# Performance work log

Measured on AMD Instinct MI355X. Metric: run time of the kernel, lower is better.

Reference implementation:

```python
import jax, jax.numpy as jnp
import numpy as np

B, S, D, H, E, TOPK = 8, 1024, 512, 2048, 8, 2


def setup_inputs() -> dict:
    key = jax.random.key(0)
    ks = jax.random.split(key, 7)
    scale = 0.02
    return {
        "x": jax.random.normal(ks[0], (B, S, D), jnp.float32),
        "gate_w": jax.random.normal(ks[1], (D, E), jnp.float32) * scale,
        "gate_b": jnp.zeros((E,), jnp.float32),
        "w1": jax.random.normal(ks[2], (E, D, H), jnp.float32) * scale,
        "b1": jnp.zeros((E, H), jnp.float32),
        "w2": jax.random.normal(ks[3], (E, H, D), jnp.float32) * scale,
        "b2": jnp.zeros((E, D), jnp.float32),
    }


def reference(x, gate_w, gate_b, w1, b1, w2, b2):
    # ---- MoE transformer MLP (fastmoe FMoETransformerMLP, NaiveGate) ----
    xt = x.reshape(-1, D)                       # [T, D], T = B*S tokens
    logits = xt @ gate_w + gate_b               # [T, E]
    top_val, top_idx = jax.lax.top_k(logits, TOPK)  # [T, k]
    score = jax.nn.softmax(top_val, axis=-1)    # softmax over the k selected logits

    y = jnp.zeros_like(xt)
    # Loop over the small fixed expert set; each token's combine weight for
    # expert e is the sum of its top-k scores routed to e (0 if not selected).
    for e in range(E):
        w_tok = jnp.sum(score * (top_idx == e), axis=-1)        # [T]
        h = jax.nn.gelu(xt @ w1[e] + b1[e], approximate=False)  # [T, H]
        y = y + w_tok[:, None] * (h @ w2[e] + b2[e])            # [T, D]

    y = y.reshape(B, S, D)
    # Outer model: log_softmax over seq of channel-summed features
    return jax.nn.log_softmax(jnp.sum(y, axis=2), axis=1)       # [B, S]
```

## Files before the change

kernel.cpp:

```cpp
#include <hip/hip_runtime.h>
#include <hip/hip_bf16.h>
#include <math.h>

#define T_TOK 8192
#define DIM   512
#define NEXP  8
#define HID   2048
#define NBAT  8
#define SEQ   1024

typedef short  short8 __attribute__((ext_vector_type(8)));
typedef float  f32x4  __attribute__((ext_vector_type(4)));

__device__ __forceinline__ unsigned short f2bf(float f) {
    union { float f; unsigned int u; } v; v.f = f;
    unsigned int u = v.u;
    unsigned int r = u + 0x7FFFu + ((u >> 16) & 1u);
    return (unsigned short)(r >> 16);
}

__device__ __forceinline__ float gelu_f(float v) {
    float v2 = v * v;
    float w = v * (-2.302344f - 0.102955f * v2);
    return v / (1.f + __builtin_amdgcn_exp2f(w));
}

__global__ void prep_gate_k(const float* __restrict__ w1, unsigned short* __restrict__ w1f,
                            const float* __restrict__ w2, const float* __restrict__ b2,
                            float* __restrict__ w2sum, float* __restrict__ b2sum,
                            int* __restrict__ counts,
                            const float* __restrict__ x, const float* __restrict__ gw,
                            const float* __restrict__ gb,
                            unsigned short* __restrict__ xb,
                            int* __restrict__ eidx, float* __restrict__ esc0,
                            float* __restrict__ esc1) {
    int bid = blockIdx.x;
    int tid = threadIdx.x;
    int wave = tid >> 6, lane = tid & 63;
    if (bid < 2048) {
        __shared__ unsigned short tile[64][68];
        int e = bid >> 8, r = bid & 255;
        int d0 = (r & 7) * 64, h0 = (r >> 3) * 64;
        const float* src = w1 + (size_t)e * DIM * HID;
        #pragma unroll
        for (int pass = 0; pass < 4; ++pass) {
            int dr = pass * 16 + (tid >> 4);
            int hc = (tid & 15) * 4;
            float4 v = *(const float4*)(src + (size_t)(d0 + dr) * HID + h0 + hc);
            tile[hc + 0][dr] = f2bf(v.x);
            tile[hc + 1][dr] = f2bf(v.y);
            tile[hc + 2][dr] = f2bf(v.z);
            tile[hc + 3][dr] = f2bf(v.w);
        }
        __syncthreads();
        int l = tid & 63, q = l >> 4, c = l & 15;
        int kk0 = (r & 7) * 2, g0 = (r >> 3) * 4;
        #pragma unroll
        for (int pi = 0; pi < 2; ++pi) {
            int sub = pi * 4 + wave;
            int kk2 = sub >> 2, g2 = sub & 3;
            const unsigned short* tp = &tile[g2 * 16 + c][kk2 * 32 + q * 8];
            ushort4 a = *(const ushort4*)(tp);
            ushort4 b = *(const ushort4*)(tp + 4);
            unsigned short* dst = w1f +
                ((size_t)(e * 128 + g0 + g2) * 16 + kk0 + kk2) * 512 + l * 8;
            *(ushort4*)(dst)     = a;
            *(ushort4*)(dst + 4) = b;
        }
    } else if (bid < 4096) {
        int t = (bid - 2048) * 4 + wave;
        const float* xp = x + (size_t)t * DIM;
        unsigned short* xbp = xb + (size_t)t * DIM;
        float acc[8] = {0, 0, 0, 0, 0, 0, 0, 0};
        #pragma unroll
        for (int it = 0; it < 8; ++it) {
            int d = it * 64 + lane;
            float xv = xp[d];
            xbp[d] = f2bf(xv);
            float4 g0 = *(const float4*)(gw + d * 8);
            float4 g1 = *(const float4*)(gw + d * 8 + 4);
            acc[0] += xv * g0.x; acc[1] += xv * g0.y; acc[2] += xv * g0.z; acc[3] += xv * g0.w;
            acc[4] += xv * g1.x; acc[5] += xv * g1.y; acc[6] += xv * g1.z; acc[7] += xv * g1.w;
        }
        #pragma unroll
        for (int e = 0; e < 8; ++e) {
            float s = acc[e];
            #pragma unroll
            for (int off = 32; off >= 1; off >>= 1) s += __shfl_xor(s, off);
            acc[e] = s + gb[e];
        }
        float v0 = -1e30f, v1 = -1e30f; int i0 = 0, i1 = 0;
        #pragma unroll
        for (int e = 0; e < 8; ++e) {
            float v = acc[e];
            if (v > v0) { v1 = v0; i1 = i0; v0 = v; i0 = e; }
            else if (v > v1) { v1 = v; i1 = e; }
        }
        float e1 = expf(v1 - v0);
        float inv = 1.f / (1.f + e1);
        if (lane == 0) {
            eidx[t] = i0 | (i1 << 4);
            esc0[t] = inv;
            esc1[t] = e1 * inv;
        }
    } else if (bid < 8192) {
        int row = (bid - 4096) * 4 + wave;
        const float* p = w2 + (size_t)row * DIM;
        float4 a = *(const float4*)(p + lane * 4);
        float4 b = *(const float4*)(p + 256 + lane * 4);
        float s = a.x + a.y + a.z + a.w + b.x + b.y + b.z + b.w;
        #pragma unroll
        for (int off = 32; off >= 1; off >>= 1) s += __shfl_xor(s, off);
        if (lane == 0) w2sum[row] = s;
    } else {
        if (tid < 8) counts[tid] = 0;
        for (int r = wave; r < NEXP; r += 4) {
            const float* p = b2 + (size_t)r * DIM;
            float s = 0.f;
            for (int i = lane; i < DIM; i += 64) s += p[i];
            #pragma unroll
            for (int off = 32; off >= 1; off >>= 1) s += __shfl_xor(s, off);
            if (lane == 0) b2sum[r] = s;
        }
    }
}

__global__ __launch_bounds__(1024) void route_k(
    const int* __restrict__ eidx, const float* __restrict__ esc0,
    const float* __restrict__ esc1, const float* __restrict__ b2sum,
    int* __restrict__ counts,
    int* __restrict__ ptok, float* __restrict__ pscore,
    float* __restrict__ s_partial) {
    int tid = threadIdx.x;
    int t = blockIdx.x * 1024 + tid;
    int wv = tid >> 6, lane = tid & 63;
    int pk = eidx[t];
    int i0 = pk & 0xf, i1 = (pk >> 4) & 0xf;
    float s0 = esc0[t], s1 = esc1[t];

    s_partial[t] = s0 * b2sum[i0] + s1 * b2sum[i1];

    __shared__ int waveCnt[16][8];
    __shared__ int waveBase[16][8];

    unsigned long long m0[8], m1[8];
    #pragma unroll
    for (int e = 0; e < 8; ++e) {
        m0[e] = __ballot(i0 == e);
        m1[e] = __ballot(i1 == e);
    }
    if (lane < 8) {
        int c = 0;
        #pragma unroll
        for (int e = 0; e < 8; ++e)
            if (lane == e) c = __popcll(m0[e]) + __popcll(m1[e]);
        waveCnt[wv][lane] = c;
    }
    __syncthreads();
    if (tid < 8) {
        int e = tid;
        int total = 0;
        #pragma unroll
        for (int w = 0; w < 16; ++w) total += waveCnt[w][e];
        int base = atomicAdd(&counts[e], total);
        int run = base;
        #pragma unroll
        for (int w = 0; w < 16; ++w) {
            waveBase[w][e] = run;
            run += waveCnt[w][e];
        }
    }
    __syncthreads();

    unsigned long long lt = (1ULL << lane) - 1ULL;
    int slot0 = 0, slot1 = 0;
    #pragma unroll
    for (int e = 0; e < 8; ++e) {
        if (i0 == e) slot0 = waveBase[wv][e] + __popcll(m0[e] & lt);
        if (i1 == e) slot1 = waveBase[wv][e] + __popcll(m0[e]) + __popcll(m1[e] & lt);
    }
    ptok[i0 * T_TOK + slot0] = t;  pscore[i0 * T_TOK + slot0] = s0;
    ptok[i1 * T_TOK + slot1] = t;  pscore[i1 * T_TOK + slot1] = s1;
}

#define GPTR(p) (const __attribute__((address_space(1))) void*)(p)
#define LPTR(p) (__attribute__((address_space(3))) void*)(p)

__global__ __launch_bounds__(256, 3) void moe_gemm_k(
    const unsigned short* __restrict__ xb, const unsigned short* __restrict__ w1f,
    const float* __restrict__ b1, const float* __restrict__ w2sum,
    const int* __restrict__ counts, const int* __restrict__ ptok,
    const float* __restrict__ pscore, float* __restrict__ s_partial) {

    int flat = blockIdx.x + (int)blockIdx.y * 135;
    int xcd = flat & 7;
    int s = flat >> 3;
    int bx = s >> 1;
    int hBase = (xcd * 2 + (s & 1)) * 128;

    int e = 8, rowBase = 0, accT = 0;
    #pragma unroll
    for (int i = 0; i < 8; ++i) {
        int nt = (counts[i] + 127) >> 7;
        if (e == 8 && bx < accT + nt) { e = i; rowBase = (bx - accT) * 128; }
        accT += nt;
    }
    if (e == 8) return;
    int n_e = counts[e];

    __shared__ unsigned short A_s[2][128 * 64];
    __shared__ int   tokLds[128];
    __shared__ float scoreLds[128];

    int tid = threadIdx.x;
    int wave = tid >> 6, lane = tid & 63;

    if (tid < 128) {
        int r = rowBase + tid;
        bool valid = r < n_e;
        tokLds[tid]   = valid ? ptok[e * T_TOK + r]   : 0;
        scoreLds[tid] = valid ? pscore[e * T_TOK + r] : 0.f;
    }
    __syncthreads();

    unsigned gAo[4];
    #pragma unroll
    for (int i = 0; i < 4; ++i) {
        int c = i * 256 + tid;
        int row = c >> 3, pos = c & 7;
        int j = (pos ^ (row & 7)) * 8;
        gAo[i] = (unsigned)tokLds[row] * DIM + j;
    }

    int wm = wave >> 1, wn = wave & 1;
    int quad = lane >> 4, col = lane & 15;

    f32x4 acc[4][4];
    #pragma unroll
    for (int m = 0; m < 4; ++m)
        #pragma unroll
        for (int n = 0; n < 4; ++n)
            acc[m][n] = (f32x4){0.f, 0.f, 0.f, 0.f};

    int aOff0 = (wm * 64 + col) * 64 + ((((0 << 2) | quad) ^ (col & 7)) * 8);
    int aOff1 = (wm * 64 + col) * 64 + ((((1 << 2) | quad) ^ (col & 7)) * 8);

    const unsigned short* bp = w1f +
        (size_t)(e * 128 + (hBase >> 4) + wn * 4) * 8192 + lane * 8;
    short8 bf0[4], bf1[4];

    #pragma unroll
    for (int i = 0; i < 4; ++i)
        __builtin_amdgcn_global_load_lds(GPTR(xb + gAo[i]), LPTR(&A_s[0][i * 2048 + tid * 8]), 16, 0, 0);
    __builtin_amdgcn_sched_barrier(0);
    #pragma unroll
    for (int i = 0; i < 4; ++i)
        __builtin_amdgcn_global_load_lds(GPTR(xb + gAo[i] + 64), LPTR(&A_s[1][i * 2048 + tid * 8]), 16, 0, 0);
    __builtin_amdgcn_sched_barrier(0);
    #pragma unroll
    for (int n = 0; n < 4; ++n) bf0[n] = *(const short8*)(bp + n * 8192);
    __builtin_amdgcn_sched_barrier(0);

    #pragma unroll
    for (int kk = 0; kk < 8; ++kk) {
        const int cur = kk & 1;
        if (kk == 0)      { asm volatile("s_waitcnt vmcnt(8)"  ::: "memory"); }
        else if (kk == 7) { asm volatile("s_waitcnt vmcnt(12)" ::: "memory"); }
        else              { asm volatile("s_waitcnt vmcnt(16)" ::: "memory"); }
        __builtin_amdgcn_s_barrier();

        #pragma unroll
        for (int n = 0; n < 4; ++n)
            bf1[n] = *(const short8*)(bp + (2 * kk + 1) * 512 + n * 8192);

        short8 af0[4], af1[4];
        const unsigned short* aB = &A_s[cur][0];
        #pragma unroll
        for (int m = 0; m < 4; ++m) af0[m] = *(const short8*)(aB + aOff0 + m * 1024);
        #pragma unroll
        for (int m = 0; m < 4; ++m) af1[m] = *(const short8*)(aB + aOff1 + m * 1024);
        asm volatile("s_waitcnt lgkmcnt(0)" ::: "memory");
        __builtin_amdgcn_s_barrier();

        if (kk < 6) {
            int ko = (kk + 2) * 64;
            #pragma unroll
            for (int i = 0; i < 4; ++i)
                __builtin_amdgcn_global_load_lds(GPTR(xb + gAo[i] + ko), LPTR(&A_s[cur][i * 2048 + tid * 8]), 16, 0, 0);
        }
        __builtin_amdgcn_sched_barrier(0);

        __builtin_amdgcn_s_setprio(1);
        #pragma unroll
        for (int m = 0; m < 4; ++m)
            #pragma unroll
            for (int n = 0; n < 4; ++n)
                acc[m][n] = __builtin_amdgcn_mfma_f32_16x16x32_bf16(af0[m], bf0[n], acc[m][n], 0, 0, 0);
        __builtin_amdgcn_s_setprio(0);

        if (kk < 7) {
            #pragma unroll
            for (int n = 0; n < 4; ++n)
                bf0[n] = *(const short8*)(bp + (2 * kk + 2) * 512 + n * 8192);
        }
        __builtin_amdgcn_sched_barrier(0);

        __builtin_amdgcn_s_setprio(1);
        #pragma unroll
        for (int m = 0; m < 4; ++m)
            #pragma unroll
            for (int n = 0; n < 4; ++n)
                acc[m][n] = __builtin_amdgcn_mfma_f32_16x16x32_bf16(af1[m], bf1[n], acc[m][n], 0, 0, 0);
        __builtin_amdgcn_s_setprio(0);
    }

    const float* b1e = b1 + e * HID;
    const float* w2e = w2sum + e * HID;
    float bias[4], wsum[4];
    #pragma unroll
    for (int n = 0; n < 4; ++n) {
        int h = hBase + wn * 64 + n * 16 + col;
        bias[n] = b1e[h];
        wsum[n] = w2e[h];
    }
    #pragma unroll
    for (int m = 0; m < 4; ++m) {
        float rp0 = 0.f, rp1 = 0.f, rp2 = 0.f, rp3 = 0.f;
        #pragma unroll
        for (int n = 0; n < 4; ++n) {
            rp0 += gelu_f(acc[m][n][0] + bias[n]) * wsum[n];
            rp1 += gelu_f(acc[m][n][1] + bias[n]) * wsum[n];
            rp2 += gelu_f(acc[m][n][2] + bias[n]) * wsum[n];
            rp3 += gelu_f(acc[m][n][3] + bias[n]) * wsum[n];
        }
        #pragma unroll
        for (int off = 8; off >= 1; off >>= 1) {
            rp0 += __shfl_xor(rp0, off);
            rp1 += __shfl_xor(rp1, off);
            rp2 += __shfl_xor(rp2, off);
            rp3 += __shfl_xor(rp3, off);
        }
        if (col < 4) {
            float mine = (col == 0) ? rp0 : (col == 1) ? rp1 : (col == 2) ? rp2 : rp3;
            int rl = wm * 64 + m * 16 + quad * 4 + col;
            int r = rowBase + rl;
            if (r < n_e)
                atomicAdd(&s_partial[tokLds[rl]], scoreLds[rl] * mine);
        }
    }
}

__global__ void lsm_k(const float* __restrict__ s, float* __restrict__ out) {
    int b = blockIdx.x, tid = threadIdx.x;
    int wave = tid >> 6, lane = tid & 63;
    __shared__ float red[4];
    const float* sp = s + (size_t)b * SEQ;
    float v[4];
    #pragma unroll
    for (int i = 0; i < 4; ++i) v[i] = sp[tid + i * 256];
    float m = fmaxf(fmaxf(v[0], v[1]), fmaxf(v[2], v[3]));
    #pragma unroll
    for (int off = 32; off >= 1; off >>= 1) m = fmaxf(m, __shfl_xor(m, off));
    if (lane == 0) red[wave] = m;
    __syncthreads();
    m = fmaxf(fmaxf(red[0], red[1]), fmaxf(red[2], red[3]));
    __syncthreads();
    float t = 0.f;
    #pragma unroll
    for (int i = 0; i < 4; ++i) t += expf(v[i] - m);
    #pragma unroll
    for (int off = 32; off >= 1; off >>= 1) t += __shfl_xor(t, off);
    if (lane == 0) red[wave] = t;
    __syncthreads();
    t = red[0] + red[1] + red[2] + red[3];
    float L = m + logf(t);
    #pragma unroll
    for (int i = 0; i < 4; ++i) out[(size_t)b * SEQ + tid + i * 256] = v[i] - L;
}

extern "C" void kernel_launch(void* const* d_in, const int* in_sizes, int n_in,
                              void* d_out, int out_size, void* d_ws, size_t ws_size,
                              hipStream_t stream) {
    const float* x  = (const float*)d_in[0];
    const float* gw = (const float*)d_in[1];
    const float* gb = (const float*)d_in[2];
    const float* w1 = (const float*)d_in[3];
    const float* b1 = (const float*)d_in[4];
    const float* w2 = (const float*)d_in[5];
    const float* b2 = (const float*)d_in[6];
    float* out = (float*)d_out;

    char* ws = (char*)d_ws;
    int*   counts    = (int*)  (ws + 0);
    float* b2sum     = (float*)(ws + 1280);
    float* s_partial = (float*)(ws + 1536);
    float* w2sum     = (float*)(ws + 34304);
    int*   ptok      = (int*)  (ws + 99840);
    float* pscore    = (float*)(ws + 361984);
    int*   eidx      = (int*)  (ws + 624128);
    float* esc0      = (float*)(ws + 656896);
    float* esc1      = (float*)(ws + 689664);
    unsigned short* xb  = (unsigned short*)(ws + 722432);
    unsigned short* w1f = (unsigned short*)(ws + 9111040);

    prep_gate_k<<<8193, 256, 0, stream>>>(w1, w1f, w2, b2, w2sum, b2sum, counts,
                                          x, gw, gb, xb, eidx, esc0, esc1);
    route_k<<<NEXP, 1024, 0, stream>>>(eidx, esc0, esc1, b2sum, counts, ptok, pscore, s_partial);
    moe_gemm_k<<<dim3(135, 16), 256, 0, stream>>>(xb, w1f, b1, w2sum, counts, ptok, pscore, s_partial);
    lsm_k<<<NBAT, 256, 0, stream>>>(s_partial, out);
}
```

Baseline: 182.0 us.

## Retile MoE GEMM waves to 128x32, vectorize gate loads, shrink route blocks

Three independent changes. The GEMM wave layout goes from a 2x2 grid of 64x64 tiles to four waves that each cover all 128 rows and 32 hidden columns. This halves the per-wave B-fragment global loads but doubles the A-fragment LDS reads. The gating kernel now reads x as float4 and writes bf16 as ushort4, cutting scalar memory ops. The routing kernel uses 32 blocks of 256 threads instead of 8 of 1024, which spreads the work across more CUs at the cost of more atomics on the expert counters.

```diff
diff --git a/kernel.cpp b/kernel.cpp
--- a/kernel.cpp
+++ b/kernel.cpp
@@ -73,14 +73,20 @@
         unsigned short* xbp = xb + (size_t)t * DIM;
         float acc[8] = {0, 0, 0, 0, 0, 0, 0, 0};
         #pragma unroll
-        for (int it = 0; it < 8; ++it) {
-            int d = it * 64 + lane;
-            float xv = xp[d];
-            xbp[d] = f2bf(xv);
-            float4 g0 = *(const float4*)(gw + d * 8);
-            float4 g1 = *(const float4*)(gw + d * 8 + 4);
-            acc[0] += xv * g0.x; acc[1] += xv * g0.y; acc[2] += xv * g0.z; acc[3] += xv * g0.w;
-            acc[4] += xv * g1.x; acc[5] += xv * g1.y; acc[6] += xv * g1.z; acc[7] += xv * g1.w;
+        for (int it = 0; it < 2; ++it) {
+            int d = it * 256 + lane * 4;
+            float4 xv = *(const float4*)(xp + d);
+            ushort4 xo;
+            xo.x = f2bf(xv.x); xo.y = f2bf(xv.y); xo.z = f2bf(xv.z); xo.w = f2bf(xv.w);
+            *(ushort4*)(xbp + d) = xo;
+            #pragma unroll
+            for (int jj = 0; jj < 4; ++jj) {
+                float xs = (jj == 0) ? xv.x : (jj == 1) ? xv.y : (jj == 2) ? xv.z : xv.w;
+                float4 g0 = *(const float4*)(gw + (d + jj) * 8);
+                float4 g1 = *(const float4*)(gw + (d + jj) * 8 + 4);
+                acc[0] += xs * g0.x; acc[1] += xs * g0.y; acc[2] += xs * g0.z; acc[3] += xs * g0.w;
+                acc[4] += xs * g1.x; acc[5] += xs * g1.y; acc[6] += xs * g1.z; acc[7] += xs * g1.w;
+            }
         }
         #pragma unroll
         for (int e = 0; e < 8; ++e) {
@@ -125,14 +131,14 @@
     }
 }
 
-__global__ __launch_bounds__(1024) void route_k(
+__global__ __launch_bounds__(256) void route_k(
     const int* __restrict__ eidx, const float* __restrict__ esc0,
     const float* __restrict__ esc1, const float* __restrict__ b2sum,
     int* __restrict__ counts,
     int* __restrict__ ptok, float* __restrict__ pscore,
     float* __restrict__ s_partial) {
     int tid = threadIdx.x;
-    int t = blockIdx.x * 1024 + tid;
+    int t = blockIdx.x * 256 + tid;
     int wv = tid >> 6, lane = tid & 63;
     int pk = eidx[t];
     int i0 = pk & 0xf, i1 = (pk >> 4) & 0xf;
@@ -140,8 +146,8 @@
 
     s_partial[t] = s0 * b2sum[i0] + s1 * b2sum[i1];
 
-    __shared__ int waveCnt[16][8];
-    __shared__ int waveBase[16][8];
+    __shared__ int waveCnt[4][8];
+    __shared__ int waveBase[4][8];
 
     unsigned long long m0[8], m1[8];
     #pragma unroll
@@ -161,11 +167,11 @@
         int e = tid;
         int total = 0;
         #pragma unroll
-        for (int w = 0; w < 16; ++w) total += waveCnt[w][e];
+        for (int w = 0; w < 4; ++w) total += waveCnt[w][e];
         int base = atomicAdd(&counts[e], total);
         int run = base;
         #pragma unroll
-        for (int w = 0; w < 16; ++w) {
+        for (int w = 0; w < 4; ++w) {
             waveBase[w][e] = run;
             run += waveCnt[w][e];
         }
@@ -232,22 +238,21 @@
         gAo[i] = (unsigned)tokLds[row] * DIM + j;
     }
 
-    int wm = wave >> 1, wn = wave & 1;
     int quad = lane >> 4, col = lane & 15;
 
-    f32x4 acc[4][4];
-    #pragma unroll
-    for (int m = 0; m < 4; ++m)
-        #pragma unroll
-        for (int n = 0; n < 4; ++n)
+    f32x4 acc[8][2];
+    #pragma unroll
+    for (int m = 0; m < 8; ++m)
+        #pragma unroll
+        for (int n = 0; n < 2; ++n)
             acc[m][n] = (f32x4){0.f, 0.f, 0.f, 0.f};
 
-    int aOff0 = (wm * 64 + col) * 64 + ((((0 << 2) | quad) ^ (col & 7)) * 8);
-    int aOff1 = (wm * 64 + col) * 64 + ((((1 << 2) | quad) ^ (col & 7)) * 8);
+    int aOff0 = col * 64 + (((0 << 2) | quad) ^ (col & 7)) * 8;
+    int aOff1 = col * 64 + (((1 << 2) | quad) ^ (col & 7)) * 8;
 
     const unsigned short* bp = w1f +
-        (size_t)(e * 128 + (hBase >> 4) + wn * 4) * 8192 + lane * 8;
-    short8 bf0[4], bf1[4];
+        (size_t)(e * 128 + (hBase >> 4) + wave * 2) * 8192 + lane * 8;
+    short8 bf0[2], bf1[2];
 
     #pragma unroll
     for (int i = 0; i < 4; ++i)
@@ -258,27 +263,26 @@
         __builtin_amdgcn_global_load_lds(GPTR(xb + gAo[i] + 64), LPTR(&A_s[1][i * 2048 + tid * 8]), 16, 0, 0);
     __builtin_amdgcn_sched_barrier(0);
     #pragma unroll
-    for (int n = 0; n < 4; ++n) bf0[n] = *(const short8*)(bp + n * 8192);
+    for (int n = 0; n < 2; ++n) bf0[n] = *(const short8*)(bp + n * 8192);
     __builtin_amdgcn_sched_barrier(0);
 
     #pragma unroll
     for (int kk = 0; kk < 8; ++kk) {
         const int cur = kk & 1;
-        if (kk == 0)      { asm volatile("s_waitcnt vmcnt(8)"  ::: "memory"); }
-        else if (kk == 7) { asm volatile("s_waitcnt vmcnt(12)" ::: "memory"); }
-        else              { asm volatile("s_waitcnt vmcnt(16)" ::: "memory"); }
+        if (kk == 0 || kk == 7) { asm volatile("s_waitcnt vmcnt(6)"  ::: "memory"); }
+        else                    { asm volatile("s_waitcnt vmcnt(10)" ::: "memory"); }
         __builtin_amdgcn_s_barrier();
 
         #pragma unroll
-        for (int n = 0; n < 4; ++n)
+        for (int n = 0; n < 2; ++n)
             bf1[n] = *(const short8*)(bp + (2 * kk + 1) * 512 + n * 8192);
 
-        short8 af0[4], af1[4];
+        short8 af0[8], af1[8];
         const unsigned short* aB = &A_s[cur][0];
         #pragma unroll
-        for (int m = 0; m < 4; ++m) af0[m] = *(const short8*)(aB + aOff0 + m * 1024);
-        #pragma unroll
-        for (int m = 0; m < 4; ++m) af1[m] = *(const short8*)(aB + aOff1 + m * 1024);
+        for (int m = 0; m < 8; ++m) af0[m] = *(const short8*)(aB + aOff0 + m * 1024);
+        #pragma unroll
+        for (int m = 0; m < 8; ++m) af1[m] = *(const short8*)(aB + aOff1 + m * 1024);
         asm volatile("s_waitcnt lgkmcnt(0)" ::: "memory");
         __builtin_amdgcn_s_barrier();
 
@@ -292,42 +296,42 @@
 
         __builtin_amdgcn_s_setprio(1);
         #pragma unroll
-        for (int m = 0; m < 4; ++m)
-            #pragma unroll
-            for (int n = 0; n < 4; ++n)
+        for (int m = 0; m < 8; ++m)
+            #pragma unroll
+            for (int n = 0; n < 2; ++n)
                 acc[m][n] = __builtin_amdgcn_mfma_f32_16x16x32_bf16(af0[m], bf0[n], acc[m][n], 0, 0, 0);
         __builtin_amdgcn_s_setprio(0);
 
         if (kk < 7) {
             #pragma unroll
-            for (int n = 0; n < 4; ++n)
+            for (int n = 0; n < 2; ++n)
                 bf0[n] = *(const short8*)(bp + (2 * kk + 2) * 512 + n * 8192);
         }
         __builtin_amdgcn_sched_barrier(0);
 
         __builtin_amdgcn_s_setprio(1);
         #pragma unroll
-        for (int m = 0; m < 4; ++m)
-            #pragma unroll
-            for (int n = 0; n < 4; ++n)
+        for (int m = 0; m < 8; ++m)
+            #pragma unroll
+            for (int n = 0; n < 2; ++n)
                 acc[m][n] = __builtin_amdgcn_mfma_f32_16x16x32_bf16(af1[m], bf1[n], acc[m][n], 0, 0, 0);
         __builtin_amdgcn_s_setprio(0);
     }
 
     const float* b1e = b1 + e * HID;
     const float* w2e = w2sum + e * HID;
-    float bias[4], wsum[4];
-    #pragma unroll
-    for (int n = 0; n < 4; ++n) {
-        int h = hBase + wn * 64 + n * 16 + col;
+    float bias[2], wsum[2];
+    #pragma unroll
+    for (int n = 0; n < 2; ++n) {
+        int h = hBase + wave * 32 + n * 16 + col;
         bias[n] = b1e[h];
         wsum[n] = w2e[h];
     }
     #pragma unroll
-    for (int m = 0; m < 4; ++m) {
+    for (int m = 0; m < 8; ++m) {
         float rp0 = 0.f, rp1 = 0.f, rp2 = 0.f, rp3 = 0.f;
         #pragma unroll
-        for (int n = 0; n < 4; ++n) {
+        for (int n = 0; n < 2; ++n) {
             rp0 += gelu_f(acc[m][n][0] + bias[n]) * wsum[n];
             rp1 += gelu_f(acc[m][n][1] + bias[n]) * wsum[n];
             rp2 += gelu_f(acc[m][n][2] + bias[n]) * wsum[n];
@@ -342,7 +346,7 @@
         }
         if (col < 4) {
             float mine = (col == 0) ? rp0 : (col == 1) ? rp1 : (col == 2) ? rp2 : rp3;
-            int rl = wm * 64 + m * 16 + quad * 4 + col;
+            int rl = m * 16 + quad * 4 + col;
             int r = rowBase + rl;
             if (r < n_e)
                 atomicAdd(&s_partial[tokLds[rl]], scoreLds[rl] * mine);
@@ -405,7 +409,7 @@
 
     prep_gate_k<<<8193, 256, 0, stream>>>(w1, w1f, w2, b2, w2sum, b2sum, counts,
                                           x, gw, gb, xb, eidx, esc0, esc1);
-    route_k<<<NEXP, 1024, 0, stream>>>(eidx, esc0, esc1, b2sum, counts, ptok, pscore, s_partial);
+    route_k<<<32, 256, 0, stream>>>(eidx, esc0, esc1, b2sum, counts, ptok, pscore, s_partial);
     moe_gemm_k<<<dim3(135, 16), 256, 0, stream>>>(xb, w1f, b1, w2sum, counts, ptok, pscore, s_partial);
     lsm_k<<<NBAT, 256, 0, stream>>>(s_partial, out);
 }
```

Result: slower. 198.7 us (+9.2%).
